# Optimization experiments

Hardware: AMD Instinct MI355X
Metric: run time of the kernel (lower is better)

Reference implementation:

```python
import jax, jax.numpy as jnp
import numpy as np

C = 64            # in_channels
IC = C // 2       # inter_channels (channel_rate=2)
R = 16            # reduction_ratio
EPS = 1e-5


def setup_inputs() -> dict:
    key = jax.random.key(0)
    ks = jax.random.split(key, 16)
    s = 0.05
    return {
        "x": jax.random.normal(ks[0], (16, C, 64, 25), dtype=jnp.float32),
        # 1x1 conv projections (common_v, key, query): [out, in] + bias
        "Wv": jax.random.normal(ks[1], (IC, C), dtype=jnp.float32) * s,
        "bv": jax.random.normal(ks[2], (IC,), dtype=jnp.float32) * s,
        "Wk": jax.random.normal(ks[3], (IC, C), dtype=jnp.float32) * s,
        "bk": jax.random.normal(ks[4], (IC,), dtype=jnp.float32) * s,
        "Wq": jax.random.normal(ks[5], (IC, C), dtype=jnp.float32) * s,
        "bq": jax.random.normal(ks[6], (IC,), dtype=jnp.float32) * s,
        # Trans_s: conv1x1 back to C + BatchNorm2d params (nonzero so output is non-trivial)
        "Wt": jax.random.normal(ks[7], (C, IC), dtype=jnp.float32) * s,
        "bt": jax.random.normal(ks[8], (C,), dtype=jnp.float32) * s,
        "gamma": jax.random.normal(ks[9], (C,), dtype=jnp.float32) * 0.5 + 1.0,
        "beta": jax.random.normal(ks[10], (C,), dtype=jnp.float32) * s,
        # ChannelGate MLP: Linear(C, C//R), Linear(C//R, C)
        "W1": jax.random.normal(ks[11], (C // R, C), dtype=jnp.float32) * s,
        "b1": jax.random.normal(ks[12], (C // R,), dtype=jnp.float32) * s,
        "W2": jax.random.normal(ks[13], (C, C // R), dtype=jnp.float32) * s,
        "b2": jax.random.normal(ks[14], (C,), dtype=jnp.float32) * s,
    }


def _conv1x1(x, W, b):
    # x: [N, Cin, T, V]; W: [Cout, Cin]
    return jnp.einsum('nctv,oc->notv', x, W) + b[None, :, None, None]


def reference(x, Wv, bv, Wk, bk, Wq, bq, Wt, bt, gamma, beta, W1, b1, W2, b2):
    N, Cc, T, V = x.shape
    TV = T * V
    ic = Wv.shape[0]

    v_x = _conv1x1(x, Wv, bv).reshape(N, ic, TV).transpose(0, 2, 1)  # [N, TV, ic]
    k_x = _conv1x1(x, Wk, bk).reshape(N, ic, TV).transpose(0, 2, 1)  # [N, TV, ic]
    q_x = _conv1x1(x, Wq, bq).reshape(N, ic, TV)                      # [N, ic, TV]

    # Unscaled dot-product attention over TV tokens (full [N, TV, TV] matrix)
    A = jnp.einsum('nti,nis->nts', k_x, q_x)
    attn = jax.nn.softmax(A, axis=-1)
    p = jnp.einsum('nts,nsi->nti', attn, v_x)                         # [N, TV, ic]
    p = p.transpose(0, 2, 1).reshape(N, ic, T, V)

    # Trans_s: conv1x1 + BatchNorm2d (training-mode batch statistics)
    p = _conv1x1(p, Wt, bt)
    mean = p.mean(axis=(0, 2, 3), keepdims=True)
    var = p.var(axis=(0, 2, 3), keepdims=True)
    p = (p - mean) * jax.lax.rsqrt(var + EPS)
    p = p * gamma[None, :, None, None] + beta[None, :, None, None]

    # ChannelGate (avg pool only) applied to original x
    avg = x.mean(axis=(2, 3))                                          # [N, C]
    h = jax.nn.relu(avg @ W1.T + b1)
    gate = jax.nn.sigmoid(h @ W2.T + b2)                               # [N, C]

    return gate[:, :, None, None] * p + x
```

## Files before the change

### kernel.cpp

```cpp
#include <hip/hip_runtime.h>
#include <hip/hip_bf16.h>
#include <math.h>

#define NB   16
#define CC   64
#define ICH  32
#define TV   1600
#define NTV  (NB*TV)

typedef __bf16 bf16x8 __attribute__((ext_vector_type(8)));
typedef float  f32x4  __attribute__((ext_vector_type(4)));

__global__ __launch_bounds__(256) void proj_gate_kernel(
    const float* __restrict__ x,
    const float* __restrict__ Wv, const float* __restrict__ bv,
    const float* __restrict__ Wk, const float* __restrict__ bk,
    const float* __restrict__ Wq, const float* __restrict__ bq,
    __bf16* __restrict__ Qb, __bf16* __restrict__ Kb,
    __bf16* __restrict__ VTb, float* __restrict__ AVG) {
  if (blockIdx.x >= 1200) {
    int b = blockIdx.x - 1200;
    int n = b >> 2, cq = b & 3;
    int c16 = threadIdx.x >> 4, l = threadIdx.x & 15;
    int c = cq * 16 + c16;
    const float4* xp = (const float4*)(x + ((size_t)n * CC + c) * TV) + l;
    float s = 0.f;
#pragma unroll
    for (int i = 0; i < 25; ++i) {
      float4 v = xp[i * 16];
      s += v.x + v.y + v.z + v.w;
    }
#pragma unroll
    for (int off = 8; off >= 1; off >>= 1) s += __shfl_down(s, off, 16);
    if (l == 0) AVG[n * CC + c] = s * (1.0f / (float)TV);
    return;
  }

  int tile = blockIdx.x / 12;
  int sub  = blockIdx.x % 12;
  int p = sub >> 2, og = sub & 3;
  int ob = og * 8;
  int tvIdx = tile * 256 + threadIdx.x;
  int n = tvIdx / TV, tv = tvIdx % TV;

  const float* W; const float* B;
  if (p == 0)      { W = Wv; B = bv; }
  else if (p == 1) { W = Wk; B = bk; }
  else             { W = Wq; B = bq; }

  float acc[8];
#pragma unroll
  for (int j = 0; j < 8; ++j) acc[j] = B[ob + j];

  const float* xp = x + (size_t)n * CC * TV + tv;
#pragma unroll 16
  for (int c = 0; c < CC; ++c) {
    float xc = xp[c * TV];
#pragma unroll
    for (int j = 0; j < 8; ++j)
      acc[j] = fmaf(W[(ob + j) * CC + c], xc, acc[j]);
  }

  if (p == 0) {
#pragma unroll
    for (int j = 0; j < 8; ++j)
      VTb[(n * ICH + ob + j) * TV + tv] = (__bf16)acc[j];
  } else {
    bf16x8 t;
#pragma unroll
    for (int j = 0; j < 8; ++j) t[j] = (__bf16)acc[j];
    int base = (n * TV + tv) * ICH + ob;
    if (p == 1) *(bf16x8*)(Qb + base) = t;
    else        *(bf16x8*)(Kb + base) = t;
  }
}

__global__ __launch_bounds__(256) void attn_kernel(
    const __bf16* __restrict__ Qb, const __bf16* __restrict__ Kb,
    const __bf16* __restrict__ VTb, __bf16* __restrict__ P,
    const float* __restrict__ Wt, const float* __restrict__ bt,
    float* __restrict__ GSP) {
  __shared__ __bf16 lds[4 * 4608];
  int b = blockIdx.x;
  int r8 = b & 7, qq = b >> 3;
  int n = r8 * 2 + (qq >= 50 ? 1 : 0);
  int rowTile = (qq >= 50) ? qq - 50 : qq;
  int row0 = rowTile * 32;

  int w = threadIdx.x >> 6;
  int lane = threadIdx.x & 63;
  int m = lane & 15, q = lane >> 4;

  __bf16* Pw = lds + w * 4608;

  const __bf16* Qn = Qb  + (size_t)n * TV * ICH;
  const __bf16* Kn = Kb  + (size_t)n * TV * ICH;
  const __bf16* Vn = VTb + (size_t)n * ICH * TV;

  bf16x8 aQ0 = *(const bf16x8*)(Qn + (row0 + m) * ICH + q * 8);
  bf16x8 aQ1 = *(const bf16x8*)(Qn + (row0 + 16 + m) * ICH + q * 8);

  f32x4 o00 = {0.f,0.f,0.f,0.f}, o01 = {0.f,0.f,0.f,0.f};
  f32x4 o10 = {0.f,0.f,0.f,0.f}, o11 = {0.f,0.f,0.f,0.f};
  f32x4 ls0 = {0.f,0.f,0.f,0.f}, ls1 = {0.f,0.f,0.f,0.f};
  const f32x4 zero = {0.f,0.f,0.f,0.f};

  int nch = (w == 3) ? 7 : 6;

  for (int jj = 0; jj < nch; jj += 2) {
    int sA = (4 * jj + (3 - w)) * 64;
    bool hasB = (jj + 1) < nch;
    int sB = hasB ? (4 * (jj + 1) + (3 - w)) * 64 : sA;

#pragma unroll
    for (int st = 0; st < 4; ++st) {
      bf16x8 bK = *(const bf16x8*)(Kn + (sA + st * 16 + m) * ICH + q * 8);
      f32x4 a0 = __builtin_amdgcn_mfma_f32_16x16x32_bf16(aQ0, bK, zero, 0, 0, 0);
      f32x4 a1 = __builtin_amdgcn_mfma_f32_16x16x32_bf16(aQ1, bK, zero, 0, 0, 0);
#pragma unroll
      for (int r = 0; r < 4; ++r) {
        float e0 = __expf(a0[r]); ls0[r] += e0;
        float e1 = __expf(a1[r]); ls1[r] += e1;
        Pw[(q * 4 + r) * 72 + st * 16 + m]        = (__bf16)e0;
        Pw[1152 + (q * 4 + r) * 72 + st * 16 + m] = (__bf16)e1;
      }
    }
    if (hasB) {
#pragma unroll
      for (int st = 0; st < 4; ++st) {
        bf16x8 bK = *(const bf16x8*)(Kn + (sB + st * 16 + m) * ICH + q * 8);
        f32x4 a0 = __builtin_amdgcn_mfma_f32_16x16x32_bf16(aQ0, bK, zero, 0, 0, 0);
        f32x4 a1 = __builtin_amdgcn_mfma_f32_16x16x32_bf16(aQ1, bK, zero, 0, 0, 0);
#pragma unroll
        for (int r = 0; r < 4; ++r) {
          float e0 = __expf(a0[r]); ls0[r] += e0;
          float e1 = __expf(a1[r]); ls1[r] += e1;
          Pw[2304 + (q * 4 + r) * 72 + st * 16 + m] = (__bf16)e0;
          Pw[3456 + (q * 4 + r) * 72 + st * 16 + m] = (__bf16)e1;
        }
      }
    }
    asm volatile("s_waitcnt lgkmcnt(0)" ::: "memory");
#pragma unroll
    for (int kc = 0; kc < 2; ++kc) {
      bf16x8 aP0 = *(const bf16x8*)(Pw + m * 72 + kc * 32 + q * 8);
      bf16x8 aP1 = *(const bf16x8*)(Pw + 1152 + m * 72 + kc * 32 + q * 8);
#pragma unroll
      for (int ict = 0; ict < 2; ++ict) {
        bf16x8 bV = *(const bf16x8*)(Vn + (ict * 16 + m) * TV + sA + kc * 32 + q * 8);
        if (ict == 0) {
          o00 = __builtin_amdgcn_mfma_f32_16x16x32_bf16(aP0, bV, o00, 0, 0, 0);
          o10 = __builtin_amdgcn_mfma_f32_16x16x32_bf16(aP1, bV, o10, 0, 0, 0);
        } else {
          o01 = __builtin_amdgcn_mfma_f32_16x16x32_bf16(aP0, bV, o01, 0, 0, 0);
          o11 = __builtin_amdgcn_mfma_f32_16x16x32_bf16(aP1, bV, o11, 0, 0, 0);
        }
      }
    }
    if (hasB) {
#pragma unroll
      for (int kc = 0; kc < 2; ++kc) {
        bf16x8 aP0 = *(const bf16x8*)(Pw + 2304 + m * 72 + kc * 32 + q * 8);
        bf16x8 aP1 = *(const bf16x8*)(Pw + 3456 + m * 72 + kc * 32 + q * 8);
#pragma unroll
        for (int ict = 0; ict < 2; ++ict) {
          bf16x8 bV = *(const bf16x8*)(Vn + (ict * 16 + m) * TV + sB + kc * 32 + q * 8);
          if (ict == 0) {
            o00 = __builtin_amdgcn_mfma_f32_16x16x32_bf16(aP0, bV, o00, 0, 0, 0);
            o10 = __builtin_amdgcn_mfma_f32_16x16x32_bf16(aP1, bV, o10, 0, 0, 0);
          } else {
            o01 = __builtin_amdgcn_mfma_f32_16x16x32_bf16(aP0, bV, o01, 0, 0, 0);
            o11 = __builtin_amdgcn_mfma_f32_16x16x32_bf16(aP1, bV, o11, 0, 0, 0);
          }
        }
      }
    }
  }

#pragma unroll
  for (int mask = 1; mask <= 8; mask <<= 1) {
#pragma unroll
    for (int r = 0; r < 4; ++r) {
      ls0[r] += __shfl_xor(ls0[r], mask, 64);
      ls1[r] += __shfl_xor(ls1[r], mask, 64);
    }
  }

  float* mf = (float*)lds;
  float* Pl = mf + 6144;
  float* red = mf + 7296;

  __syncthreads();
  float* mp = mf + (w * 64 + lane) * 24;
#pragma unroll
  for (int r = 0; r < 4; ++r) {
    mp[r]      = o00[r]; mp[4 + r]  = o01[r];
    mp[8 + r]  = o10[r]; mp[12 + r] = o11[r];
    mp[16 + r] = ls0[r]; mp[20 + r] = ls1[r];
  }
  __syncthreads();
  if (w == 0) {
#pragma unroll
    for (int ww = 1; ww < 4; ++ww) {
      const float* sp = mf + (ww * 64 + lane) * 24;
#pragma unroll
      for (int r = 0; r < 4; ++r) {
        o00[r] += sp[r];      o01[r] += sp[4 + r];
        o10[r] += sp[8 + r];  o11[r] += sp[12 + r];
        ls0[r] += sp[16 + r]; ls1[r] += sp[20 + r];
      }
    }
#pragma unroll
    for (int r = 0; r < 4; ++r) {
      float i0 = 1.f / ls0[r], i1 = 1.f / ls1[r];
      float p00 = o00[r] * i0, p01 = o01[r] * i0;
      float p10 = o10[r] * i1, p11 = o11[r] * i1;
      int pb0 = (n * TV + row0 + q * 4 + r) * ICH;
      int pb1 = pb0 + 16 * ICH;
      P[pb0 + m]      = (__bf16)p00;
      P[pb0 + 16 + m] = (__bf16)p01;
      P[pb1 + m]      = (__bf16)p10;
      P[pb1 + 16 + m] = (__bf16)p11;
      Pl[(q * 4 + r) * 36 + m]           = p00;
      Pl[(q * 4 + r) * 36 + 16 + m]      = p01;
      Pl[(16 + q * 4 + r) * 36 + m]      = p10;
      Pl[(16 + q * 4 + r) * 36 + 16 + m] = p11;
    }
  }
  __syncthreads();

  int c = threadIdx.x & 63;
  float wr[ICH];
#pragma unroll
  for (int i = 0; i < ICH; ++i) wr[i] = Wt[c * ICH + i];
  float bc = bt[c];
  float sy = 0.f, sy2 = 0.f;
#pragma unroll
  for (int rr = 0; rr < 8; ++rr) {
    const f32x4* pr = (const f32x4*)(Pl + (w * 8 + rr) * 36);
    float y = bc;
#pragma unroll
    for (int u = 0; u < 8; ++u) {
      f32x4 pv = pr[u];
#pragma unroll
      for (int k = 0; k < 4; ++k) y = fmaf(wr[u * 4 + k], pv[k], y);
    }
    sy += y; sy2 += y * y;
  }
  red[w * 128 + c]      = sy;
  red[w * 128 + 64 + c] = sy2;
  __syncthreads();
  if (threadIdx.x < 128) {
    int t = threadIdx.x;
    float s = red[t] + red[128 + t] + red[256 + t] + red[384 + t];
    GSP[(size_t)blockIdx.x * 128 + t] = s;
  }
}

__global__ __launch_bounds__(256) void finalize_stats(
    const float* __restrict__ GSP, const float* __restrict__ gamma,
    const float* __restrict__ beta, const float* __restrict__ AVG,
    const float* __restrict__ W1, const float* __restrict__ b1,
    const float* __restrict__ W2, const float* __restrict__ b2,
    float* __restrict__ SS, float* __restrict__ GATE) {
  int t = threadIdx.x;
  __shared__ float acc2[2][128];
  __shared__ float shs[128];
  __shared__ float sh[NB][4];
  {
    int c = t & 127, half = t >> 7;
    float s = 0.f;
    for (int b = half * 400; b < half * 400 + 400; ++b)
      s += GSP[(size_t)b * 128 + c];
    acc2[half][c] = s;
  }
  __syncthreads();
  if (t < 128) shs[t] = acc2[0][t] + acc2[1][t];
  __syncthreads();
  if (t < 64) {
    int c = t;
    float mean = shs[c] * (1.f / (float)NTV);
    float var  = shs[64 + c] * (1.f / (float)NTV) - mean * mean;
    float scale = rsqrtf(var + 1e-5f) * gamma[c];
    SS[c] = scale;
    SS[64 + c] = beta[c] - mean * scale;
    int n = t >> 2, jj = t & 3;
    float h = b1[jj];
    for (int c2 = 0; c2 < CC; ++c2)
      h = fmaf(W1[jj * CC + c2], AVG[n * CC + c2], h);
    sh[n][jj] = fmaxf(h, 0.f);
  }
  __syncthreads();
#pragma unroll
  for (int u = 0; u < 4; ++u) {
    int idx = t * 4 + u;
    int n = idx >> 6, c = idx & 63;
    float g = b2[c];
#pragma unroll
    for (int jj = 0; jj < 4; ++jj) g = fmaf(W2[c * 4 + jj], sh[n][jj], g);
    GATE[idx] = 1.f / (1.f + __expf(-g));
  }
}

__global__ __launch_bounds__(256) void apply_kernel(
    const __bf16* __restrict__ P, const float* __restrict__ Wt,
    const float* __restrict__ bt, const float* __restrict__ SS,
    const float* __restrict__ gate, const float* __restrict__ x,
    float* __restrict__ out) {
  int cg = blockIdx.x / 100;
  int tb = blockIdx.x % 100;
  int tvIdx = tb * 256 + threadIdx.x;
  int n = tvIdx / TV, tv = tvIdx % TV;

  float f[ICH];
  const bf16x8* pp = (const bf16x8*)(P + ((size_t)(n * TV + tv)) * ICH);
#pragma unroll
  for (int u = 0; u < 4; ++u) {
    bf16x8 v = pp[u];
#pragma unroll
    for (int j = 0; j < 8; ++j) f[u * 8 + j] = (float)v[j];
  }

#pragma unroll
  for (int j = 0; j < 8; ++j) {
    int c = cg * 8 + j;
    float y = bt[c];
#pragma unroll
    for (int i = 0; i < ICH; ++i) y = fmaf(Wt[c * ICH + i], f[i], y);
    size_t idx = ((size_t)(n * CC + c)) * TV + tv;
    out[idx] = gate[n * CC + c] * fmaf(y, SS[c], SS[64 + c]) + x[idx];
  }
}

extern "C" void kernel_launch(void* const* d_in, const int* in_sizes, int n_in,
                              void* d_out, int out_size, void* d_ws, size_t ws_size,
                              hipStream_t stream) {
  const float* x     = (const float*)d_in[0];
  const float* Wv    = (const float*)d_in[1];
  const float* bv    = (const float*)d_in[2];
  const float* Wk    = (const float*)d_in[3];
  const float* bk    = (const float*)d_in[4];
  const float* Wq    = (const float*)d_in[5];
  const float* bq    = (const float*)d_in[6];
  const float* Wt    = (const float*)d_in[7];
  const float* bt    = (const float*)d_in[8];
  const float* gamma = (const float*)d_in[9];
  const float* beta  = (const float*)d_in[10];
  const float* W1    = (const float*)d_in[11];
  const float* b1    = (const float*)d_in[12];
  const float* W2    = (const float*)d_in[13];
  const float* b2    = (const float*)d_in[14];
  float* out = (float*)d_out;
  char* ws = (char*)d_ws;

  const size_t E = 819200;
  __bf16* Qb  = (__bf16*)(ws);
  __bf16* Kb  = (__bf16*)(ws + 2*E);
  __bf16* VTb = (__bf16*)(ws + 4*E);
  __bf16* Pb  = (__bf16*)(ws + 6*E);
  float*  GSP = (float*) (ws + 8*E);
  float*  SS  = (float*) (ws + 8*E + 409600);
  float*  GATE= (float*) (ws + 8*E + 410112);
  float*  AVG = out;

  proj_gate_kernel<<<1264, 256, 0, stream>>>(x, Wv, bv, Wk, bk, Wq, bq,
                                             Qb, Kb, VTb, AVG);
  attn_kernel<<<NB * 50, 256, 0, stream>>>(Qb, Kb, VTb, Pb, Wt, bt, GSP);
  finalize_stats<<<1, 256, 0, stream>>>(GSP, gamma, beta, AVG,
                                        W1, b1, W2, b2, SS, GATE);
  apply_kernel<<<800, 256, 0, stream>>>(Pb, Wt, bt, SS, GATE, x, out);
}
```

Measured before the change: 148.8 us.

## Process one key chunk per iteration, prefetch V, and split the cross-wave reduction across waves

```diff
diff --git a/kernel.cpp b/kernel.cpp
--- a/kernel.cpp
+++ b/kernel.cpp
@@ -80,7 +80,7 @@
     const __bf16* __restrict__ VTb, __bf16* __restrict__ P,
     const float* __restrict__ Wt, const float* __restrict__ bt,
     float* __restrict__ GSP) {
-  __shared__ __bf16 lds[4 * 4608];
+  __shared__ float smem_f[7936];
   int b = blockIdx.x;
   int r8 = b & 7, qq = b >> 3;
   int n = r8 * 2 + (qq >= 50 ? 1 : 0);
@@ -91,7 +91,7 @@
   int lane = threadIdx.x & 63;
   int m = lane & 15, q = lane >> 4;
 
-  __bf16* Pw = lds + w * 4608;
+  __bf16* Pw = (__bf16*)smem_f + w * 2304;
 
   const __bf16* Qn = Qb  + (size_t)n * TV * ICH;
   const __bf16* Kn = Kb  + (size_t)n * TV * ICH;
@@ -107,14 +107,11 @@
 
   int nch = (w == 3) ? 7 : 6;
 
-  for (int jj = 0; jj < nch; jj += 2) {
-    int sA = (4 * jj + (3 - w)) * 64;
-    bool hasB = (jj + 1) < nch;
-    int sB = hasB ? (4 * (jj + 1) + (3 - w)) * 64 : sA;
-
+  for (int j = 0; j < nch; ++j) {
+    int s0 = (4 * j + (3 - w)) * 64;
 #pragma unroll
     for (int st = 0; st < 4; ++st) {
-      bf16x8 bK = *(const bf16x8*)(Kn + (sA + st * 16 + m) * ICH + q * 8);
+      bf16x8 bK = *(const bf16x8*)(Kn + (s0 + st * 16 + m) * ICH + q * 8);
       f32x4 a0 = __builtin_amdgcn_mfma_f32_16x16x32_bf16(aQ0, bK, zero, 0, 0, 0);
       f32x4 a1 = __builtin_amdgcn_mfma_f32_16x16x32_bf16(aQ1, bK, zero, 0, 0, 0);
 #pragma unroll
@@ -125,55 +122,21 @@
         Pw[1152 + (q * 4 + r) * 72 + st * 16 + m] = (__bf16)e1;
       }
     }
-    if (hasB) {
-#pragma unroll
-      for (int st = 0; st < 4; ++st) {
-        bf16x8 bK = *(const bf16x8*)(Kn + (sB + st * 16 + m) * ICH + q * 8);
-        f32x4 a0 = __builtin_amdgcn_mfma_f32_16x16x32_bf16(aQ0, bK, zero, 0, 0, 0);
-        f32x4 a1 = __builtin_amdgcn_mfma_f32_16x16x32_bf16(aQ1, bK, zero, 0, 0, 0);
-#pragma unroll
-        for (int r = 0; r < 4; ++r) {
-          float e0 = __expf(a0[r]); ls0[r] += e0;
-          float e1 = __expf(a1[r]); ls1[r] += e1;
-          Pw[2304 + (q * 4 + r) * 72 + st * 16 + m] = (__bf16)e0;
-          Pw[3456 + (q * 4 + r) * 72 + st * 16 + m] = (__bf16)e1;
-        }
-      }
-    }
+    bf16x8 pV[2][2];
+#pragma unroll
+    for (int kc = 0; kc < 2; ++kc)
+#pragma unroll
+      for (int ict = 0; ict < 2; ++ict)
+        pV[kc][ict] = *(const bf16x8*)(Vn + (ict * 16 + m) * TV + s0 + kc * 32 + q * 8);
     asm volatile("s_waitcnt lgkmcnt(0)" ::: "memory");
 #pragma unroll
     for (int kc = 0; kc < 2; ++kc) {
       bf16x8 aP0 = *(const bf16x8*)(Pw + m * 72 + kc * 32 + q * 8);
       bf16x8 aP1 = *(const bf16x8*)(Pw + 1152 + m * 72 + kc * 32 + q * 8);
-#pragma unroll
-      for (int ict = 0; ict < 2; ++ict) {
-        bf16x8 bV = *(const bf16x8*)(Vn + (ict * 16 + m) * TV + sA + kc * 32 + q * 8);
-        if (ict == 0) {
-          o00 = __builtin_amdgcn_mfma_f32_16x16x32_bf16(aP0, bV, o00, 0, 0, 0);
-          o10 = __builtin_amdgcn_mfma_f32_16x16x32_bf16(aP1, bV, o10, 0, 0, 0);
-        } else {
-          o01 = __builtin_amdgcn_mfma_f32_16x16x32_bf16(aP0, bV, o01, 0, 0, 0);
-          o11 = __builtin_amdgcn_mfma_f32_16x16x32_bf16(aP1, bV, o11, 0, 0, 0);
-        }
-      }
-    }
-    if (hasB) {
-#pragma unroll
-      for (int kc = 0; kc < 2; ++kc) {
-        bf16x8 aP0 = *(const bf16x8*)(Pw + 2304 + m * 72 + kc * 32 + q * 8);
-        bf16x8 aP1 = *(const bf16x8*)(Pw + 3456 + m * 72 + kc * 32 + q * 8);
-#pragma unroll
-        for (int ict = 0; ict < 2; ++ict) {
-          bf16x8 bV = *(const bf16x8*)(Vn + (ict * 16 + m) * TV + sB + kc * 32 + q * 8);
-          if (ict == 0) {
-            o00 = __builtin_amdgcn_mfma_f32_16x16x32_bf16(aP0, bV, o00, 0, 0, 0);
-            o10 = __builtin_amdgcn_mfma_f32_16x16x32_bf16(aP1, bV, o10, 0, 0, 0);
-          } else {
-            o01 = __builtin_amdgcn_mfma_f32_16x16x32_bf16(aP0, bV, o01, 0, 0, 0);
-            o11 = __builtin_amdgcn_mfma_f32_16x16x32_bf16(aP1, bV, o11, 0, 0, 0);
-          }
-        }
-      }
+      o00 = __builtin_amdgcn_mfma_f32_16x16x32_bf16(aP0, pV[kc][0], o00, 0, 0, 0);
+      o10 = __builtin_amdgcn_mfma_f32_16x16x32_bf16(aP1, pV[kc][0], o10, 0, 0, 0);
+      o01 = __builtin_amdgcn_mfma_f32_16x16x32_bf16(aP0, pV[kc][1], o01, 0, 0, 0);
+      o11 = __builtin_amdgcn_mfma_f32_16x16x32_bf16(aP1, pV[kc][1], o11, 0, 0, 0);
     }
   }
 
@@ -186,45 +149,35 @@
     }
   }
 
-  float* mf = (float*)lds;
-  float* Pl = mf + 6144;
-  float* red = mf + 7296;
-
-  __syncthreads();
-  float* mp = mf + (w * 64 + lane) * 24;
-#pragma unroll
-  for (int r = 0; r < 4; ++r) {
-    mp[r]      = o00[r]; mp[4 + r]  = o01[r];
-    mp[8 + r]  = o10[r]; mp[12 + r] = o11[r];
-    mp[16 + r] = ls0[r]; mp[20 + r] = ls1[r];
-  }
-  __syncthreads();
-  if (w == 0) {
+  float* pub = smem_f;
+  float* Pl  = smem_f + 6144;
+  float* red = smem_f + 7296;
+
+  __syncthreads();
+  f32x4* mp = (f32x4*)(pub + (w * 64 + lane) * 24);
+  mp[0] = o00; mp[1] = o01; mp[2] = o10; mp[3] = o11;
+  mp[4] = ls0; mp[5] = ls1;
+  __syncthreads();
+
+  {
+    int lsIdx = 4 + (w >> 1);
+    const f32x4* p0 = (const f32x4*)(pub + lane * 24);
+    f32x4 osum = p0[w];
+    f32x4 lsum = p0[lsIdx];
 #pragma unroll
     for (int ww = 1; ww < 4; ++ww) {
-      const float* sp = mf + (ww * 64 + lane) * 24;
-#pragma unroll
-      for (int r = 0; r < 4; ++r) {
-        o00[r] += sp[r];      o01[r] += sp[4 + r];
-        o10[r] += sp[8 + r];  o11[r] += sp[12 + r];
-        ls0[r] += sp[16 + r]; ls1[r] += sp[20 + r];
-      }
-    }
+      const f32x4* pp = (const f32x4*)(pub + (ww * 64 + lane) * 24);
+      f32x4 ov = pp[w], lv = pp[lsIdx];
+#pragma unroll
+      for (int r = 0; r < 4; ++r) { osum[r] += ov[r]; lsum[r] += lv[r]; }
+    }
+    int tile = w >> 1, colh = (w & 1) * 16;
 #pragma unroll
     for (int r = 0; r < 4; ++r) {
-      float i0 = 1.f / ls0[r], i1 = 1.f / ls1[r];
-      float p00 = o00[r] * i0, p01 = o01[r] * i0;
-      float p10 = o10[r] * i1, p11 = o11[r] * i1;
-      int pb0 = (n * TV + row0 + q * 4 + r) * ICH;
-      int pb1 = pb0 + 16 * ICH;
-      P[pb0 + m]      = (__bf16)p00;
-      P[pb0 + 16 + m] = (__bf16)p01;
-      P[pb1 + m]      = (__bf16)p10;
-      P[pb1 + 16 + m] = (__bf16)p11;
-      Pl[(q * 4 + r) * 36 + m]           = p00;
-      Pl[(q * 4 + r) * 36 + 16 + m]      = p01;
-      Pl[(16 + q * 4 + r) * 36 + m]      = p10;
-      Pl[(16 + q * 4 + r) * 36 + 16 + m] = p11;
+      float p = osum[r] / lsum[r];
+      int row = tile * 16 + q * 4 + r;
+      P[(n * TV + row0 + row) * ICH + colh + m] = (__bf16)p;
+      Pl[row * 36 + colh + m] = p;
     }
   }
   __syncthreads();
```

After: 142.7 us. 1.04x faster.
